# Optimization experiments

Hardware: AMD Instinct MI355X
Metric: run time of the kernel (lower is better)

Reference implementation:

```python
import jax, jax.numpy as jnp
import numpy as np

N_NODES = 100000


def gcn_conv(x, edge_index, W, b):
    """PyG-style GCNConv: h = D^-1/2 (A+I) D^-1/2 (x W) + b."""
    n = x.shape[0]
    loop = jnp.arange(n)
    src = jnp.concatenate([edge_index[0], loop])  # [E+N]
    dst = jnp.concatenate([edge_index[1], loop])  # [E+N]
    # degree computed on destination nodes (PyG gcn_norm with self-loops)
    deg = jnp.zeros((n,), x.dtype).at[dst].add(1.0)
    dinv = jnp.where(deg > 0, jax.lax.rsqrt(deg), 0.0)
    norm = dinv[src] * dinv[dst]  # [E+N]
    h = x @ W  # [n, out]
    msg = h[src] * norm[:, None]  # gather + scale
    out = jax.ops.segment_sum(msg, dst, num_segments=n)  # scatter-add
    return out + b


def setup_inputs() -> dict:
    key = jax.random.key(0)
    ks = jax.random.split(key, 8)
    F_in, H, C = 64, 64, 32
    x = jax.random.normal(ks[0], (N_NODES, F_in), dtype=jnp.float32)
    edge_index = jax.random.randint(ks[1], (2, 1200000), 0, N_NODES, dtype=jnp.int64)
    W1 = jax.random.normal(ks[2], (F_in, H), dtype=jnp.float32) / np.sqrt(F_in)
    b1 = jnp.zeros((H,), jnp.float32)
    W2 = jax.random.normal(ks[3], (H, H), dtype=jnp.float32) / np.sqrt(H)
    b2 = jnp.zeros((H,), jnp.float32)
    Wc = jax.random.normal(ks[4], (H, C), dtype=jnp.float32) / np.sqrt(H)
    bc = jnp.zeros((C,), jnp.float32)
    return {"x": x, "edge_index": edge_index, "W1": W1, "b1": b1,
            "W2": W2, "b2": b2, "Wc": Wc, "bc": bc}


def reference(x, edge_index, W1, b1, W2, b2, Wc, bc):
    h = jnp.tanh(gcn_conv(x, edge_index, W1, b1))
    h = jnp.tanh(gcn_conv(h, edge_index, W2, b2))
    out = h @ Wc + bc
    return (out, h)
```

## Files before the change

kernel.cpp:

```cpp
#include <hip/hip_runtime.h>
#include <hip/hip_bf16.h>
#include <stdint.h>

#define CB_SHIFT 8
#define CB_NODES 256
#define CAP 3584
#define NBINS 512
#define PT 4096

static __device__ inline uint16_t f2bf(float f) {
    union { float f; uint32_t u; } v; v.f = f;
    uint32_t r = v.u + 0x7FFFu + ((v.u >> 16) & 1u);
    return (uint16_t)(r >> 16);
}
static __device__ inline float bflo(uint32_t u) {
    union { uint32_t u; float f; } v; v.u = u << 16; return v.f;
}
static __device__ inline float bfhi(uint32_t u) {
    union { uint32_t u; float f; } v; v.u = u & 0xFFFF0000u; return v.f;
}
static __device__ inline float bfu(uint16_t u) {
    union { uint32_t u; float f; } v; v.u = ((uint32_t)u) << 16; return v.f;
}
static __device__ inline float tanh_fast(float x) {
    x = fminf(fmaxf(x, -20.f), 20.f);
    float e = __expf(2.f * x);
    return fmaf(-2.f, __builtin_amdgcn_rcpf(e + 1.f), 1.f);
}

__global__ __launch_bounds__(256) void k_init(const uint32_t* __restrict__ e, int E,
                                              int* __restrict__ flag, int* __restrict__ gcur,
                                              int* __restrict__ dhist) {
    int t = threadIdx.x;
    dhist[t] = 0;
    gcur[t] = 0;
    gcur[256 + t] = 0;
    if (t < 64) {
        int cnt = E < 1024 ? E : 1024;
        int nz = 0;
        for (int i = t; i < cnt; i += 64) nz |= (e[2 * i + 1] != 0u);
        int any = __any(nz);
        if (t == 0) *flag = any ? 0 : 1;
    }
}

__global__ __launch_bounds__(512) void k_part(const uint32_t* __restrict__ e, int E,
                                              const int* __restrict__ flag,
                                              int* __restrict__ gcur,
                                              uint32_t* __restrict__ parts) {
    __shared__ int sh_hist[NBINS], sh_off[NBINS], sh_base[NBINS], pw[8];
    __shared__ uint32_t sh_buf[PT];
    __shared__ uint16_t sh_bkt[PT];
    int t = threadIdx.x;
    int tile0 = blockIdx.x * PT;
    int is64 = *flag;
    sh_hist[t] = 0;
    __syncthreads();

    uint32_t rec[8]; int cb[8], rank[8];
    const uint2* e2p = (const uint2*)e;
#pragma unroll
    for (int j = 0; j < 8; ++j) {
        int idx = tile0 + j * 512 + t;
        cb[j] = -1;
        if (idx < E) {
            uint32_t s, d;
            if (is64) { s = e2p[idx].x; d = e2p[E + idx].x; }
            else      { s = e[idx];     d = e[E + idx]; }
            rec[j] = (s << CB_SHIFT) | (d & (CB_NODES - 1));
            cb[j] = (int)(d >> CB_SHIFT);
            rank[j] = atomicAdd(&sh_hist[cb[j]], 1);
        }
    }
    __syncthreads();
    int c = sh_hist[t];
    int lane = t & 63, w = t >> 6;
    int incl = c;
    for (int o = 1; o < 64; o <<= 1) {
        int v = __shfl_up(incl, o);
        if (lane >= o) incl += v;
    }
    if (lane == 63) pw[w] = incl;
    __syncthreads();
    if (t < 8) {
        int v = pw[t];
        int inc2 = v;
#pragma unroll
        for (int o = 1; o < 8; o <<= 1) {
            int u = __shfl_up(inc2, o);
            if (t >= o) inc2 += u;
        }
        pw[t] = inc2 - v;
    }
    __syncthreads();
    {
        int ex = pw[w] + incl - c;
        sh_off[t] = ex;
        sh_base[t] = c ? atomicAdd(&gcur[t], c) : 0;
    }
    __syncthreads();
#pragma unroll
    for (int j = 0; j < 8; ++j) {
        if (cb[j] >= 0) {
            int slot = sh_off[cb[j]] + rank[j];
            sh_buf[slot] = rec[j];
            sh_bkt[slot] = (uint16_t)cb[j];
        }
    }
    __syncthreads();
    int total = min(PT, E - tile0);
    for (int i = t; i < total; i += 512) {
        int b = sh_bkt[i];
        int dest = sh_base[b] + (i - sh_off[b]);
        parts[(size_t)b * CAP + dest] = sh_buf[i];
    }
}

__global__ __launch_bounds__(512) void k_build(const uint32_t* __restrict__ parts,
                                               const int* __restrict__ gcur,
                                               float* __restrict__ dinv,
                                               int* __restrict__ rowbeg,
                                               int* __restrict__ rowend,
                                               uint32_t* __restrict__ col,
                                               int* __restrict__ dhist, int N) {
    __shared__ int hist[CB_NODES], cur[CB_NODES], dh[256], wsum4[4];
    __shared__ uint32_t sbuf[CAP];
    int t = threadIdx.x, cb = blockIdx.x;
    if (t < 256) { hist[t] = 0; dh[t] = 0; }
    __syncthreads();
    int cnt = gcur[cb];
    const uint32_t* rp = parts + (size_t)cb * CAP;
    for (int i = t; i < cnt; i += 512) atomicAdd(&hist[rp[i] & (CB_NODES - 1)], 1);
    __syncthreads();
    int h = 0, incl = 0;
    if (t < 256) {
        h = hist[t];
        int lane = t & 63;
        incl = h;
        for (int o = 1; o < 64; o <<= 1) {
            int v = __shfl_up(incl, o);
            if (lane >= o) incl += v;
        }
        if (lane == 63) wsum4[t >> 6] = incl;
    }
    __syncthreads();
    if (t == 0) {
        int r = 0;
        for (int k = 0; k < 4; ++k) { int v = wsum4[k]; wsum4[k] = r; r += v; }
    }
    __syncthreads();
    if (t < 256) {
        int ex = wsum4[t >> 6] + incl - h;
        cur[t] = ex;
        int n = cb * CB_NODES + t;
        int base = cb * CAP;
        if (n < N) {
            rowbeg[n] = base + ex;
            rowend[n] = base + ex + h;
            dinv[n] = rsqrtf((float)(h + 1));
            atomicAdd(&dh[min(h, 255)], 1);
        }
    }
    __syncthreads();
    if (t < 256 && dh[t]) atomicAdd(&dhist[t], dh[t]);
    for (int i = t; i < cnt; i += 512) {
        uint32_t rec = rp[i];
        int pos = atomicAdd(&cur[rec & (CB_NODES - 1)], 1);
        sbuf[pos] = rec >> CB_SHIFT;
    }
    __syncthreads();
    int base = cb * CAP;
    for (int i = t; i < cnt; i += 512) col[base + i] = sbuf[i];
}

__global__ __launch_bounds__(256) void k_dscan(const int* __restrict__ dhist,
                                               int* __restrict__ dcur) {
    __shared__ int sd[256];
    int t = threadIdx.x;
    int v = dhist[t];
    sd[t] = v; __syncthreads();
    for (int o = 1; o < 256; o <<= 1) {
        int x = (t >= o) ? sd[t - o] : 0;
        __syncthreads();
        sd[t] += x;
        __syncthreads();
    }
    dcur[t] = sd[t] - v;
}

__global__ __launch_bounds__(1024) void k_dperm(const int* __restrict__ rowbeg,
                                                const int* __restrict__ rowend,
                                                const float* __restrict__ dinv,
                                                int* __restrict__ dcur,
                                                int4* __restrict__ perm4, int N) {
    __shared__ int lh[256], lbase[256];
    int t = threadIdx.x;
    if (t < 256) lh[t] = 0;
    __syncthreads();
    int n = blockIdx.x * 1024 + t;
    int c = 0, rank = 0, beg = 0, deg = 0;
    if (n < N) {
        beg = rowbeg[n];
        deg = rowend[n] - beg;
        c = min(deg, 255);
        rank = atomicAdd(&lh[c], 1);
    }
    __syncthreads();
    if (t < 256 && lh[t]) lbase[t] = atomicAdd(&dcur[t], lh[t]);
    __syncthreads();
    if (n < N) {
        int pos = lbase[c] + rank;
        perm4[(N - 1) - pos] = make_int4(beg, deg, n, __float_as_int(dinv[n]));
    }
}

template<int ABF16>
__global__ __launch_bounds__(256) void k_gemm(const void* __restrict__ Ap,
                                              const float* __restrict__ W,
                                              const float* __restrict__ dinv,
                                              uint16_t* __restrict__ out, int N) {
    __shared__ __align__(16) float xT[64 * 68];
    __shared__ __align__(16) float Wl[64 * 64];
    int t = threadIdx.x;
#pragma unroll
    for (int j = 0; j < 16; ++j) Wl[j * 256 + t] = W[j * 256 + t];
    int n0 = blockIdx.x * 64;
    int nvalid = min(64, N - n0);
#pragma unroll
    for (int j = 0; j < 4; ++j) {
        int flat = j * 256 + t;
        int node = flat >> 4;
        int k4 = (flat & 15) * 4;
        float4 v = make_float4(0.f, 0.f, 0.f, 0.f);
        if (node < nvalid) {
            if (ABF16) {
                ushort4 u = *((const ushort4*)Ap + ((size_t)(n0 + node) * 16 + (k4 >> 2)));
                v = make_float4(bfu(u.x), bfu(u.y), bfu(u.z), bfu(u.w));
            } else {
                v = *(const float4*)((const float*)Ap + (size_t)(n0 + node) * 64 + k4);
            }
        }
        xT[(k4 + 0) * 68 + node] = v.x;
        xT[(k4 + 1) * 68 + node] = v.y;
        xT[(k4 + 2) * 68 + node] = v.z;
        xT[(k4 + 3) * 68 + node] = v.w;
    }
    __syncthreads();
    int ng = t >> 4, cg = t & 15;
    float acc[4][4] = {};
#pragma unroll 8
    for (int k = 0; k < 64; ++k) {
        float4 a = *(const float4*)&xT[k * 68 + 4 * ng];
        float4 b = *(const float4*)&Wl[k * 64 + 4 * cg];
        float av[4] = {a.x, a.y, a.z, a.w};
        float bv[4] = {b.x, b.y, b.z, b.w};
#pragma unroll
        for (int i = 0; i < 4; ++i)
#pragma unroll
            for (int j = 0; j < 4; ++j) acc[i][j] = fmaf(av[i], bv[j], acc[i][j]);
    }
#pragma unroll
    for (int i = 0; i < 4; ++i) {
        int ln = 4 * ng + i;
        if (ln < nvalid) {
            int n = n0 + ln;
            float dv = dinv[n];
            ushort4 o;
            o.x = f2bf(acc[i][0] * dv);
            o.y = f2bf(acc[i][1] * dv);
            o.z = f2bf(acc[i][2] * dv);
            o.w = f2bf(acc[i][3] * dv);
            *(ushort4*)&out[(size_t)n * 64 + 4 * cg] = o;
        }
    }
}

template<int OBF16, int CLS>
__global__ __launch_bounds__(512) void k_agg(const uint16_t* __restrict__ h,
                                             const int4* __restrict__ perm4,
                                             const uint32_t* __restrict__ col,
                                             const float* __restrict__ bias,
                                             void* __restrict__ out,
                                             const float* __restrict__ Wc,
                                             const float* __restrict__ bc,
                                             float* __restrict__ outc, int N) {
    __shared__ __align__(16) float WcL[CLS ? 64 * 32 : 1];
    __shared__ __align__(16) float hstage[CLS ? 8 : 1][4][64];
    int t = threadIdx.x;
    if (CLS) {
#pragma unroll
        for (int j = 0; j < 4; ++j) WcL[j * 512 + t] = Wc[j * 512 + t];
        __syncthreads();
    }
    int lane = t & 63, wid = t >> 6;
    int sub  = (lane >> 3) & 1;
    int g = lane & 7;
    const uint4* hp = (const uint4*)h;
    float bv[4];
#pragma unroll
    for (int j = 0; j < 4; ++j) bv[j] = bias[g * 8 + sub * 4 + j];
    int slot = lane >> 4;
    int idx = (blockIdx.x * 8 + wid) * 4 + slot;
    bool valid = idx < N;
    int4 pi = make_int4(0, 0, 0, 0);
    if (valid) pi = perm4[idx];
    int rs = pi.x, deg = valid ? pi.y : 0, n = pi.z;
    float di = __int_as_float(pi.w);
    int m = deg;
#pragma unroll
    for (int o = 1; o < 64; o <<= 1) m = max(m, __shfl_xor(m, o));
    int trips = (m + 1) >> 1;
    float acc[8] = {};
#pragma unroll 8
    for (int it = 0; it < trips; ++it) {
        int e = 2 * it + sub;
        if (e < deg) {
            int src = (int)col[rs + e];
            uint4 v = hp[(size_t)src * 8 + g];
            acc[0] += bflo(v.x); acc[1] += bfhi(v.x);
            acc[2] += bflo(v.y); acc[3] += bfhi(v.y);
            acc[4] += bflo(v.z); acc[5] += bfhi(v.z);
            acc[6] += bflo(v.w); acc[7] += bfhi(v.w);
        }
    }
#pragma unroll
    for (int j = 0; j < 8; ++j) acc[j] += __shfl_xor(acc[j], 8);
    if (valid) {
        float s0 = sub ? acc[4] : acc[0];
        float s1 = sub ? acc[5] : acc[1];
        float s2 = sub ? acc[6] : acc[2];
        float s3 = sub ? acc[7] : acc[3];
        uint2 v = *(const uint2*)&h[(size_t)n * 64 + g * 8 + sub * 4];
        float hn0 = bflo(v.x), hn1 = bfhi(v.x), hn2 = bflo(v.y), hn3 = bfhi(v.y);
        float r0 = tanh_fast(di * (s0 + hn0) + bv[0]);
        float r1 = tanh_fast(di * (s1 + hn1) + bv[1]);
        float r2 = tanh_fast(di * (s2 + hn2) + bv[2]);
        float r3 = tanh_fast(di * (s3 + hn3) + bv[3]);
        if (OBF16) {
            ushort4 ob;
            ob.x = f2bf(r0); ob.y = f2bf(r1); ob.z = f2bf(r2); ob.w = f2bf(r3);
            *(ushort4*)&((uint16_t*)out)[(size_t)n * 64 + g * 8 + sub * 4] = ob;
        } else {
            __align__(16) float o[4] = {r0, r1, r2, r3};
            *(float4*)&((float*)out)[(size_t)n * 64 + g * 8 + sub * 4] = *(float4*)&o[0];
        }
        if (CLS)
            *(float4*)&hstage[wid][slot][g * 8 + sub * 4] = make_float4(r0, r1, r2, r3);
    }
    if (CLS) {
        int q = lane & 15;
        if (valid) {
            float a0 = 0.f, a1 = 0.f;
#pragma unroll
            for (int k = 0; k < 64; k += 4) {
                float4 hv = *(const float4*)&hstage[wid][slot][k];
                float2 w0 = *(const float2*)&WcL[(k + 0) * 32 + 2 * q];
                float2 w1 = *(const float2*)&WcL[(k + 1) * 32 + 2 * q];
                float2 w2 = *(const float2*)&WcL[(k + 2) * 32 + 2 * q];
                float2 w3 = *(const float2*)&WcL[(k + 3) * 32 + 2 * q];
                a0 = fmaf(hv.x, w0.x, a0); a1 = fmaf(hv.x, w0.y, a1);
                a0 = fmaf(hv.y, w1.x, a0); a1 = fmaf(hv.y, w1.y, a1);
                a0 = fmaf(hv.z, w2.x, a0); a1 = fmaf(hv.z, w2.y, a1);
                a0 = fmaf(hv.w, w3.x, a0); a1 = fmaf(hv.w, w3.y, a1);
            }
            float2 bcv = *(const float2*)&bc[2 * q];
            float2 o = make_float2(a0 + bcv.x, a1 + bcv.y);
            *(float2*)&outc[(size_t)n * 32 + 2 * q] = o;
        }
    }
}

extern "C" void kernel_launch(void* const* d_in, const int* in_sizes, int n_in,
                              void* d_out, int out_size, void* d_ws, size_t ws_size,
                              hipStream_t stream) {
    const float*    x     = (const float*)d_in[0];
    const uint32_t* edges = (const uint32_t*)d_in[1];
    const float*    W1    = (const float*)d_in[2];
    const float*    b1    = (const float*)d_in[3];
    const float*    W2    = (const float*)d_in[4];
    const float*    b2    = (const float*)d_in[5];
    const float*    Wc    = (const float*)d_in[6];
    const float*    bc    = (const float*)d_in[7];

    const int N   = in_sizes[0] / 64;
    const int E   = in_sizes[1] / 2;
    const int NBC = (N + CB_NODES - 1) >> CB_SHIFT;
    const int NTG = (N + 63) / 64;
    const int NTP = (E + PT - 1) / PT;
    const int NAG = (N + 31) / 32;
    const int NDP = (N + 1023) / 1024;

    char* w = (char*)d_ws;
    size_t off = 0;
    auto alloc = [&](size_t bytes) {
        void* p = w + off;
        off = (off + bytes + 255) & ~(size_t)255;
        return p;
    };
    int*      flag   = (int*)alloc(4);
    int*      gcur   = (int*)alloc(NBINS * 4);
    int*      dhist  = (int*)alloc(256 * 4);
    int*      dcur   = (int*)alloc(256 * 4);
    float*    dinv   = (float*)alloc((size_t)N * 4);
    uint32_t* parts  = (uint32_t*)alloc((size_t)NBC * CAP * 4);
    uint32_t* col    = (uint32_t*)alloc((size_t)NBC * CAP * 4);
    int*      rowbeg = (int*)alloc((size_t)N * 4);
    int*      rowend = (int*)alloc((size_t)N * 4);
    uint16_t* bufA   = (uint16_t*)alloc((size_t)N * 64 * 2);
    uint16_t* bufB   = (uint16_t*)alloc((size_t)N * 64 * 2);
    int4*     perm4  = (int4*)parts;

    float* outc = (float*)d_out;
    float* hfin = outc + (size_t)N * 32;

    hipLaunchKernelGGL(k_init, dim3(1), dim3(256), 0, stream, edges, E, flag, gcur, dhist);
    hipLaunchKernelGGL(k_part, dim3(NTP), dim3(512), 0, stream, edges, E, flag, gcur, parts);
    hipLaunchKernelGGL(k_build, dim3(NBC), dim3(512), 0, stream, parts, gcur, dinv, rowbeg, rowend, col, dhist, N);
    hipLaunchKernelGGL(k_dscan, dim3(1), dim3(256), 0, stream, dhist, dcur);
    hipLaunchKernelGGL(k_dperm, dim3(NDP), dim3(1024), 0, stream, rowbeg, rowend, dinv, dcur, perm4, N);

    hipLaunchKernelGGL(HIP_KERNEL_NAME(k_gemm<0>), dim3(NTG), dim3(256), 0, stream,
                       (const void*)x, W1, dinv, bufA, N);
    hipLaunchKernelGGL(HIP_KERNEL_NAME(k_agg<1, 0>), dim3(NAG), dim3(512), 0, stream,
                       bufA, perm4, col, b1, (void*)bufB, (const float*)nullptr,
                       (const float*)nullptr, (float*)nullptr, N);
    hipLaunchKernelGGL(HIP_KERNEL_NAME(k_gemm<1>), dim3(NTG), dim3(256), 0, stream,
                       (const void*)bufB, W2, dinv, bufA, N);
    hipLaunchKernelGGL(HIP_KERNEL_NAME(k_agg<0, 1>), dim3(NAG), dim3(512), 0, stream,
                       bufA, perm4, col, b2, (void*)hfin, Wc, bc, outc, N);
}
```

Baseline: 236.2 us.

## Drop degree-sorted node permutation and write per-node records directly in build

Removes the degree histogram, its scan kernel and the degree-bucketed permutation kernel; k_build now writes the per-node int4 record (row start, degree, node, dinv) in natural node order. This saves two kernel launches and the rowbeg/rowend round trip, but aggregation waves no longer see nodes grouped by similar degree, which can raise intra-wave load imbalance. It also pads the classifier staging buffer row to 68 floats to reduce LDS bank conflicts, and gives perm4 its own allocation instead of aliasing parts.

```diff
diff --git a/kernel.cpp b/kernel.cpp
--- a/kernel.cpp
+++ b/kernel.cpp
@@ -29,10 +29,8 @@
 }
 
 __global__ __launch_bounds__(256) void k_init(const uint32_t* __restrict__ e, int E,
-                                              int* __restrict__ flag, int* __restrict__ gcur,
-                                              int* __restrict__ dhist) {
+                                              int* __restrict__ flag, int* __restrict__ gcur) {
     int t = threadIdx.x;
-    dhist[t] = 0;
     gcur[t] = 0;
     gcur[256 + t] = 0;
     if (t < 64) {
@@ -119,14 +117,12 @@
 __global__ __launch_bounds__(512) void k_build(const uint32_t* __restrict__ parts,
                                                const int* __restrict__ gcur,
                                                float* __restrict__ dinv,
-                                               int* __restrict__ rowbeg,
-                                               int* __restrict__ rowend,
-                                               uint32_t* __restrict__ col,
-                                               int* __restrict__ dhist, int N) {
-    __shared__ int hist[CB_NODES], cur[CB_NODES], dh[256], wsum4[4];
+                                               int4* __restrict__ perm4,
+                                               uint32_t* __restrict__ col, int N) {
+    __shared__ int hist[CB_NODES], cur[CB_NODES], wsum4[4];
     __shared__ uint32_t sbuf[CAP];
     int t = threadIdx.x, cb = blockIdx.x;
-    if (t < 256) { hist[t] = 0; dh[t] = 0; }
+    if (t < 256) hist[t] = 0;
     __syncthreads();
     int cnt = gcur[cb];
     const uint32_t* rp = parts + (size_t)cb * CAP;
@@ -155,14 +151,12 @@
         int n = cb * CB_NODES + t;
         int base = cb * CAP;
         if (n < N) {
-            rowbeg[n] = base + ex;
-            rowend[n] = base + ex + h;
-            dinv[n] = rsqrtf((float)(h + 1));
-            atomicAdd(&dh[min(h, 255)], 1);
-        }
-    }
-    __syncthreads();
-    if (t < 256 && dh[t]) atomicAdd(&dhist[t], dh[t]);
+            float dv = rsqrtf((float)(h + 1));
+            dinv[n] = dv;
+            perm4[n] = make_int4(base + ex, h, n, __float_as_int(dv));
+        }
+    }
+    __syncthreads();
     for (int i = t; i < cnt; i += 512) {
         uint32_t rec = rp[i];
         int pos = atomicAdd(&cur[rec & (CB_NODES - 1)], 1);
@@ -171,47 +165,6 @@
     __syncthreads();
     int base = cb * CAP;
     for (int i = t; i < cnt; i += 512) col[base + i] = sbuf[i];
-}
-
-__global__ __launch_bounds__(256) void k_dscan(const int* __restrict__ dhist,
-                                               int* __restrict__ dcur) {
-    __shared__ int sd[256];
-    int t = threadIdx.x;
-    int v = dhist[t];
-    sd[t] = v; __syncthreads();
-    for (int o = 1; o < 256; o <<= 1) {
-        int x = (t >= o) ? sd[t - o] : 0;
-        __syncthreads();
-        sd[t] += x;
-        __syncthreads();
-    }
-    dcur[t] = sd[t] - v;
-}
-
-__global__ __launch_bounds__(1024) void k_dperm(const int* __restrict__ rowbeg,
-                                                const int* __restrict__ rowend,
-                                                const float* __restrict__ dinv,
-                                                int* __restrict__ dcur,
-                                                int4* __restrict__ perm4, int N) {
-    __shared__ int lh[256], lbase[256];
-    int t = threadIdx.x;
-    if (t < 256) lh[t] = 0;
-    __syncthreads();
-    int n = blockIdx.x * 1024 + t;
-    int c = 0, rank = 0, beg = 0, deg = 0;
-    if (n < N) {
-        beg = rowbeg[n];
-        deg = rowend[n] - beg;
-        c = min(deg, 255);
-        rank = atomicAdd(&lh[c], 1);
-    }
-    __syncthreads();
-    if (t < 256 && lh[t]) lbase[t] = atomicAdd(&dcur[t], lh[t]);
-    __syncthreads();
-    if (n < N) {
-        int pos = lbase[c] + rank;
-        perm4[(N - 1) - pos] = make_int4(beg, deg, n, __float_as_int(dinv[n]));
-    }
 }
 
 template<int ABF16>
@@ -285,7 +238,7 @@
                                              const float* __restrict__ bc,
                                              float* __restrict__ outc, int N) {
     __shared__ __align__(16) float WcL[CLS ? 64 * 32 : 1];
-    __shared__ __align__(16) float hstage[CLS ? 8 : 1][4][64];
+    __shared__ __align__(16) float hstage[CLS ? 8 : 1][4][68];
     int t = threadIdx.x;
     if (CLS) {
 #pragma unroll
@@ -388,7 +341,6 @@
     const int NTG = (N + 63) / 64;
     const int NTP = (E + PT - 1) / PT;
     const int NAG = (N + 31) / 32;
-    const int NDP = (N + 1023) / 1024;
 
     char* w = (char*)d_ws;
     size_t off = 0;
@@ -399,25 +351,19 @@
     };
     int*      flag   = (int*)alloc(4);
     int*      gcur   = (int*)alloc(NBINS * 4);
-    int*      dhist  = (int*)alloc(256 * 4);
-    int*      dcur   = (int*)alloc(256 * 4);
     float*    dinv   = (float*)alloc((size_t)N * 4);
     uint32_t* parts  = (uint32_t*)alloc((size_t)NBC * CAP * 4);
     uint32_t* col    = (uint32_t*)alloc((size_t)NBC * CAP * 4);
-    int*      rowbeg = (int*)alloc((size_t)N * 4);
-    int*      rowend = (int*)alloc((size_t)N * 4);
+    int4*     perm4  = (int4*)alloc((size_t)N * 16);
     uint16_t* bufA   = (uint16_t*)alloc((size_t)N * 64 * 2);
     uint16_t* bufB   = (uint16_t*)alloc((size_t)N * 64 * 2);
-    int4*     perm4  = (int4*)parts;
 
     float* outc = (float*)d_out;
     float* hfin = outc + (size_t)N * 32;
 
-    hipLaunchKernelGGL(k_init, dim3(1), dim3(256), 0, stream, edges, E, flag, gcur, dhist);
+    hipLaunchKernelGGL(k_init, dim3(1), dim3(256), 0, stream, edges, E, flag, gcur);
     hipLaunchKernelGGL(k_part, dim3(NTP), dim3(512), 0, stream, edges, E, flag, gcur, parts);
-    hipLaunchKernelGGL(k_build, dim3(NBC), dim3(512), 0, stream, parts, gcur, dinv, rowbeg, rowend, col, dhist, N);
-    hipLaunchKernelGGL(k_dscan, dim3(1), dim3(256), 0, stream, dhist, dcur);
-    hipLaunchKernelGGL(k_dperm, dim3(NDP), dim3(1024), 0, stream, rowbeg, rowend, dinv, dcur, perm4, N);
+    hipLaunchKernelGGL(k_build, dim3(NBC), dim3(512), 0, stream, parts, gcur, dinv, perm4, col, N);
 
     hipLaunchKernelGGL(HIP_KERNEL_NAME(k_gemm<0>), dim3(NTG), dim3(256), 0, stream,
                        (const void*)x, W1, dinv, bufA, N);
```

Result: no change. 233.5 us (-1.1%).
